# Kernel tuning notes

Measured on AMD Instinct MI355X. Metric: run time of the kernel, lower is better.

Reference implementation:

```python
import jax, jax.numpy as jnp
import numpy as np

B, D, N, MH, MV = 4, 1024, 2048, 1024, 1024

def setup_inputs() -> dict:
    key = jax.random.key(0)
    k1, k2, k3, k4, k5 = jax.random.split(key, 5)
    return {
        "x": jax.random.normal(k1, (B, D, N), dtype=jnp.float32),
        "W_Q": jax.random.normal(k2, (MH, D), dtype=jnp.float32),
        "W_K": jax.random.normal(k3, (MH, D), dtype=jnp.float32),
        "W_V": jax.random.normal(k4, (MV, D), dtype=jnp.float32),
        "W_O": jax.random.normal(k5, (D, MV), dtype=jnp.float32),
    }

def reference(x, W_Q, W_K, W_V, W_O):
    # x: [b, d, n] (feature-major). Projections: [b, m, n]
    q = jnp.einsum('hd,bdn->bhn', W_Q, x)
    k = jnp.einsum('hd,bdn->bhn', W_K, x)
    v = jnp.einsum('vd,bdn->bvn', W_V, x)
    # scores[b,i,j] = sum_h k[b,h,i] * q[b,h,j]  -> [b, n, n]; NOTE: no 1/sqrt scale (faithful)
    scores = jnp.einsum('bhi,bhj->bij', k, q)
    scores = jax.nn.softmax(scores, axis=-1)
    # v @ scores -> [b, m_V, n]
    attn = jnp.einsum('bvi,bij->bvj', v, scores)
    # W_O @ attn -> [b, d, n]
    return jnp.einsum('dv,bvj->bdj', W_O, attn)
```

## Files before the change

### kernel.cpp

```cpp
#include <hip/hip_runtime.h>
#include <cstddef>
#include <cstdint>

typedef unsigned short u16;
typedef __attribute__((ext_vector_type(8))) short bf16x8;
typedef __attribute__((ext_vector_type(8))) _Float16 f16x8;
typedef __attribute__((ext_vector_type(4))) float f32x4;
typedef __attribute__((ext_vector_type(16))) float f32x16;

#define GLOBAL_AS __attribute__((address_space(1)))
#define LDS_AS __attribute__((address_space(3)))

__device__ __forceinline__ void async16(const u16* g, u16* l) {
    __builtin_amdgcn_global_load_lds((GLOBAL_AS const uint32_t*)g,
                                     (LDS_AS uint32_t*)l, 16, 0, 0);
}

__device__ __forceinline__ u16 f2bf(float f) {
    uint32_t u = __builtin_bit_cast(uint32_t, f);
    uint32_t r = (u + 0x7FFFu + ((u >> 16) & 1u)) >> 16;
    return (u16)r;
}

#define VMC(N) asm volatile("s_waitcnt vmcnt(" #N ")" ::: "memory")

__global__ __launch_bounds__(256)
void wcast(const float4* __restrict__ src, u16* __restrict__ dst)
{
    int i = blockIdx.x * 256 + threadIdx.x;
    float4 v = src[i];
    ushort4 a = { f2bf(v.x), f2bf(v.y), f2bf(v.z), f2bf(v.w) };
    *(ushort4*)&dst[4 * (size_t)i] = a;
}

__global__ __launch_bounds__(256)
void tsplit_h2(const float* __restrict__ Sb, size_t sBatch,
               u16* __restrict__ Db, size_t dBatch, size_t plane,
               int R, int C)
{
    const float* S = Sb + blockIdx.z * sBatch;
    u16* D = Db + blockIdx.z * dBatch;
    __shared__ float t[32][33];
    int tx = threadIdx.x & 31, ty = threadIdx.x >> 5;
    int c0 = blockIdx.x * 32, r0 = blockIdx.y * 32;
    #pragma unroll
    for (int k = 0; k < 4; ++k)
        t[ty + 8 * k][tx] = S[(size_t)(r0 + ty + 8 * k) * C + c0 + tx];
    __syncthreads();
    #pragma unroll
    for (int k = 0; k < 4; ++k) {
        float a = t[tx][ty + 8 * k] * 64.0f;
        _Float16 h0 = (_Float16)a;
        _Float16 h1 = (_Float16)(a - (float)h0);
        size_t o = (size_t)(c0 + ty + 8 * k) * R + r0 + tx;
        D[o] = __builtin_bit_cast(u16, h0);
        D[plane + o] = __builtin_bit_cast(u16, h1);
    }
}

__global__ __launch_bounds__(256)
void xprep(const float* __restrict__ Sb, size_t sBatch,
           u16* __restrict__ BFb, size_t bfBatch,
           u16* __restrict__ Db, size_t dBatch, size_t plane)
{
    const float* S = Sb + blockIdx.z * sBatch;
    u16* BF = BFb + blockIdx.z * bfBatch;
    u16* D = Db + blockIdx.z * dBatch;
    __shared__ float t[32][33];
    int tx = threadIdx.x & 31, ty = threadIdx.x >> 5;
    int c0 = blockIdx.x * 32, r0 = blockIdx.y * 32;
    #pragma unroll
    for (int k = 0; k < 4; ++k) {
        float v = S[(size_t)(r0 + ty + 8 * k) * 2048 + c0 + tx];
        t[ty + 8 * k][tx] = v;
        BF[(size_t)(r0 + ty + 8 * k) * 2048 + c0 + tx] = f2bf(v);
    }
    __syncthreads();
    #pragma unroll
    for (int k = 0; k < 4; ++k) {
        float a = t[tx][ty + 8 * k] * 64.0f;
        _Float16 h0 = (_Float16)a;
        _Float16 h1 = (_Float16)(a - (float)h0);
        size_t o = (size_t)(c0 + ty + 8 * k) * 1024 + r0 + tx;
        D[o] = __builtin_bit_cast(u16, h0);
        D[plane + o] = __builtin_bit_cast(u16, h1);
    }
}

__global__ __launch_bounds__(256)
void tcast(const float* __restrict__ S, u16* __restrict__ D, int R, int C)
{
    __shared__ float t[32][33];
    int tx = threadIdx.x & 31, ty = threadIdx.x >> 5;
    int c0 = blockIdx.x * 32, r0 = blockIdx.y * 32;
    #pragma unroll
    for (int k = 0; k < 4; ++k)
        t[ty + 8 * k][tx] = S[(size_t)(r0 + ty + 8 * k) * C + c0 + tx];
    __syncthreads();
    #pragma unroll
    for (int k = 0; k < 4; ++k)
        D[(size_t)(c0 + ty + 8 * k) * R + r0 + tx] = f2bf(t[tx][ty + 8 * k]);
}

__global__ __launch_bounds__(256)
void tbf16(const u16* __restrict__ Sb, size_t sBatch, u16* __restrict__ Db, size_t dBatch)
{
    const u16* S = Sb + blockIdx.z * sBatch;
    u16* D = Db + blockIdx.z * dBatch;
    __shared__ u16 t[32][34];
    int tx = threadIdx.x & 31, ty = threadIdx.x >> 5;
    int c0 = blockIdx.x * 32, r0 = blockIdx.y * 32;
    #pragma unroll
    for (int k = 0; k < 4; ++k)
        t[ty + 8 * k][tx] = S[(size_t)(r0 + ty + 8 * k) * 2048 + c0 + tx];
    __syncthreads();
    #pragma unroll
    for (int k = 0; k < 4; ++k)
        D[(size_t)(c0 + ty + 8 * k) * 2048 + r0 + tx] = t[tx][ty + 8 * k];
}

#define MMF4(AF, BF)                                                                   \
    _Pragma("unroll") for (int i = 0; i < 4; ++i)                                      \
        _Pragma("unroll") for (int j = 0; j < 4; ++j)                                  \
            acc[i][j] = __builtin_amdgcn_mfma_f32_16x16x32_f16(AF[i], BF[j], acc[i][j], 0, 0, 0);
#define MMB4(AF, BF)                                                                   \
    _Pragma("unroll") for (int i = 0; i < 4; ++i)                                      \
        _Pragma("unroll") for (int j = 0; j < 4; ++j)                                  \
            acc[i][j] = __builtin_amdgcn_mfma_f32_16x16x32_bf16(AF[i], BF[j], acc[i][j], 0, 0, 0);

template<int TERMS, int EPI>
__global__ __launch_bounds__(256)
void gemm_big(const u16* __restrict__ Ab, size_t aBatch, size_t aPlane,
              const u16* __restrict__ Bb, size_t bBatch, size_t bPlane,
              void* __restrict__ Cb, size_t cBatch, size_t cPlane,
              int M, int N, int K)
{
    constexpr int RSZ = 4096;
    constexpr int BUF = (TERMS == 3 ? 4 : 2) * RSZ;
    __shared__ u16 lds[2 * BUF];
    const u16* A = Ab + blockIdx.z * aBatch;
    const u16* B = Bb + blockIdx.z * bBatch;
    const int tid = threadIdx.x;
    const int lane = tid & 63, wave = tid >> 6;
    const int m0 = blockIdx.y * 128, n0 = blockIdx.x * 128;
    const int l15 = lane & 15, q = lane >> 4;
    const int rm = (wave >> 1) * 64, rn = (wave & 1) * 64;

    int sr[2], sg[2], sbase[2];
    #pragma unroll
    for (int it = 0; it < 2; ++it) {
        int s = tid + it * 256;
        sr[it] = s >> 2;
        sg[it] = (s & 3) ^ ((sr[it] >> 1) & 3);
        sbase[it] = (it * 256 + wave * 64) * 8;
    }
    const int fsw = (q ^ ((l15 >> 1) & 3)) * 8;
    int aoff[4], boff[4];
    #pragma unroll
    for (int f = 0; f < 4; ++f) {
        aoff[f] = (rm + f * 16 + l15) * 32 + fsw;
        boff[f] = (rn + f * 16 + l15) * 32 + fsw;
    }

    f32x4 acc[4][4];
    #pragma unroll
    for (int i = 0; i < 4; ++i)
        #pragma unroll
        for (int j = 0; j < 4; ++j)
            acc[i][j] = (f32x4){0.f, 0.f, 0.f, 0.f};

#define STAGEB(PP, KT)                                                                 \
    do {                                                                               \
        _Pragma("unroll")                                                              \
        for (int it = 0; it < 2; ++it) {                                               \
            const size_t ao = (size_t)(m0 + sr[it]) * K + (KT) + sg[it] * 8;           \
            const size_t bo = (size_t)(n0 + sr[it]) * K + (KT) + sg[it] * 8;           \
            const int d = (PP) * BUF + sbase[it];                                      \
            if (TERMS == 3) {                                                          \
                async16(A + ao, &lds[d]);                                              \
                async16(A + aPlane + ao, &lds[d + RSZ]);                               \
                async16(B + bo, &lds[d + 2 * RSZ]);                                    \
                async16(B + bPlane + bo, &lds[d + 3 * RSZ]);                           \
            } else {                                                                   \
                async16(A + ao, &lds[d]);                                              \
                async16(B + bo, &lds[d + RSZ]);                                        \
            }                                                                          \
        }                                                                              \
    } while (0)

    STAGEB(0, 0);
    for (int kt = 0; kt < K; kt += 32) {
        const int p = (kt >> 5) & 1;
        __syncthreads();
        if (kt + 32 < K) STAGEB(p ^ 1, kt + 32);
        const u16* L = &lds[p * BUF];
        if (TERMS == 3) {
            f16x8 a0f[4], b0f[4], xf[4];
            #pragma unroll
            for (int f = 0; f < 4; ++f) a0f[f] = *(const f16x8*)&L[aoff[f]];
            #pragma unroll
            for (int f = 0; f < 4; ++f) b0f[f] = *(const f16x8*)&L[2 * RSZ + boff[f]];
            MMF4(a0f, b0f);
            #pragma unroll
            for (int f = 0; f < 4; ++f) xf[f] = *(const f16x8*)&L[3 * RSZ + boff[f]];
            MMF4(a0f, xf);
            #pragma unroll
            for (int f = 0; f < 4; ++f) xf[f] = *(const f16x8*)&L[RSZ + aoff[f]];
            MMF4(xf, b0f);
        } else {
            bf16x8 af[4], bf_[4];
            #pragma unroll
            for (int f = 0; f < 4; ++f) af[f] = *(const bf16x8*)&L[aoff[f]];
            #pragma unroll
            for (int f = 0; f < 4; ++f) bf_[f] = *(const bf16x8*)&L[RSZ + boff[f]];
            MMB4(af, bf_);
        }
    }
#undef STAGEB

    #pragma unroll
    for (int i = 0; i < 4; ++i) {
        int row = m0 + rm + i * 16 + q * 4;
        #pragma unroll
        for (int j = 0; j < 4; ++j) {
            int col = n0 + rn + j * 16 + l15;
            #pragma unroll
            for (int r = 0; r < 4; ++r) {
                float v = acc[i][j][r];
                size_t o = (size_t)(row + r) * N + col;
                if (EPI == 0) {
                    ((float*)Cb + blockIdx.z * cBatch)[o] = v;
                } else if (EPI == 1) {
                    u16* C0 = (u16*)Cb + blockIdx.z * cBatch;
                    float vs = v * 0.000244140625f;
                    _Float16 h0 = (_Float16)vs;
                    _Float16 h1 = (_Float16)(vs - (float)h0);
                    C0[o] = __builtin_bit_cast(u16, h0);
                    C0[cPlane + o] = __builtin_bit_cast(u16, h1);
                } else {
                    ((u16*)Cb + blockIdx.z * cBatch)[o] = f2bf(v);
                }
            }
        }
    }
}

template<int TERMS, int EPI, int TM, int TN, int WGM, int WGN>
__global__ __launch_bounds__(512, 2)
void gemm_w(const u16* __restrict__ Ab, size_t aBatch, size_t aPlane,
            const u16* __restrict__ Bb, size_t bBatch, size_t bPlane,
            void* __restrict__ Cb, size_t cBatch, size_t cPlane,
            int M, int N, int K)
{
    constexpr int ASZ = TM * 32;
    constexpr int BSZ = TN * 32;
    constexpr int APL = (TERMS == 3) ? 2 : 1;
    constexpr int BUF = APL * (ASZ + BSZ);
    constexpr int FM = TM / WGM / 32;
    constexpr int FN = TN / WGN / 32;
    constexpr int AIT = TM / 128;
    constexpr int BIT = TN / 128;
    extern __shared__ __align__(16) u16 lds[];

    int bid = blockIdx.x + gridDim.x * blockIdx.y;
    int cpr = gridDim.x >> 2;
    int c8 = bid & 7, kk = bid >> 3;
    int bx = (kk % cpr) * 4 + (c8 & 3);
    int by = (kk / cpr) * 2 + (c8 >> 2);

    const u16* A = Ab + blockIdx.z * aBatch;
    const u16* B = Bb + blockIdx.z * bBatch;
    const int tid = threadIdx.x;
    const int lane = tid & 63, wave = tid >> 6;
    const int m0 = by * TM, n0 = bx * TN;
    const int l31 = lane & 31, half = lane >> 5;
    const int rm = (wave / WGN) * (TM / WGM);
    const int rn = (wave % WGN) * (TN / WGN);

    int arow[FM], asw[FM], brow[FN], bsw[FN];
    #pragma unroll
    for (int f = 0; f < FM; ++f) { arow[f] = rm + f * 32 + l31; asw[f] = (arow[f] >> 1) & 3; }
    #pragma unroll
    for (int f = 0; f < FN; ++f) { brow[f] = rn + f * 32 + l31; bsw[f] = (brow[f] >> 1) & 3; }

    f32x16 acc[FM][FN];
    #pragma unroll
    for (int i = 0; i < FM; ++i)
        #pragma unroll
        for (int j = 0; j < FN; ++j)
            #pragma unroll
            for (int r = 0; r < 16; ++r) acc[i][j][r] = 0.f;

    auto stage = [&](int pp, int kt) {
        #pragma unroll
        for (int it = 0; it < AIT; ++it) {
            int s = tid + it * 512;
            int r = s >> 2;
            int g = (s & 3) ^ ((r >> 1) & 3);
            int base = pp * BUF + (it * 512 + wave * 64) * 8;
            size_t go = (size_t)(m0 + r) * K + kt + g * 8;
            async16(A + go, &lds[base]);
            if (TERMS == 3) async16(A + aPlane + go, &lds[base + ASZ]);
        }
        #pragma unroll
        for (int it = 0; it < BIT; ++it) {
            int s = tid + it * 512;
            int r = s >> 2;
            int g = (s & 3) ^ ((r >> 1) & 3);
            int base = pp * BUF + APL * ASZ + (it * 512 + wave * 64) * 8;
            size_t go = (size_t)(n0 + r) * K + kt + g * 8;
            async16(B + go, &lds[base]);
            if (TERMS == 3) async16(B + bPlane + go, &lds[base + BSZ]);
        }
    };

    stage(0, 0);
    for (int kt = 0; kt < K; kt += 32) {
        const int p = (kt >> 5) & 1;
        __syncthreads();
        if (kt + 32 < K) stage(p ^ 1, kt + 32);
        const u16* L = &lds[p * BUF];
        #pragma unroll
        for (int h = 0; h < 2; ++h) {
            bf16x8 a0[FM], b0[FN];
            #pragma unroll
            for (int f = 0; f < FM; ++f)
                a0[f] = *(const bf16x8*)&L[arow[f] * 32 + ((2 * h + half) ^ asw[f]) * 8];
            #pragma unroll
            for (int f = 0; f < FN; ++f)
                b0[f] = *(const bf16x8*)&L[ASZ + brow[f] * 32 + ((2 * h + half) ^ bsw[f]) * 8];
            #pragma unroll
            for (int i = 0; i < FM; ++i)
                #pragma unroll
                for (int j = 0; j < FN; ++j)
                    acc[i][j] = __builtin_amdgcn_mfma_f32_32x32x16_bf16(a0[i], b0[j], acc[i][j], 0, 0, 0);
        }
    }

    #pragma unroll
    for (int i = 0; i < FM; ++i) {
        #pragma unroll
        for (int j = 0; j < FN; ++j) {
            int col = n0 + rn + j * 32 + l31;
            #pragma unroll
            for (int r = 0; r < 16; ++r) {
                int row = m0 + rm + i * 32 + (r & 3) + 8 * (r >> 2) + 4 * half;
                float v = acc[i][j][r];
                size_t o = (size_t)row * N + col;
                if (EPI == 0) {
                    ((float*)Cb + blockIdx.z * cBatch)[o] = v;
                } else if (EPI == 1) {
                    u16* C0 = (u16*)Cb + blockIdx.z * cBatch;
                    float vs = v * 0.000244140625f;
                    _Float16 h0 = (_Float16)vs;
                    _Float16 h1 = (_Float16)(vs - (float)h0);
                    C0[o] = __builtin_bit_cast(u16, h0);
                    C0[cPlane + o] = __builtin_bit_cast(u16, h1);
                } else {
                    ((u16*)Cb + blockIdx.z * cBatch)[o] = f2bf(v);
                }
            }
        }
    }
}

template<int EPI, int TM, int TN, int WGM, int WGN>
__global__ __launch_bounds__(512, 2)
void gemm_p6(const u16* __restrict__ Ab, size_t aBatch, size_t aPlane,
             const u16* __restrict__ Bb, size_t bBatch, size_t bPlane,
             void* __restrict__ Cb, size_t cBatch, size_t cPlane,
             int M, int N, int K)
{
    constexpr int ASZ = TM * 32;
    constexpr int BSZ = TN * 32;
    constexpr int BUFU = 2 * (ASZ + BSZ);
    constexpr int FM = TM / WGM / 32;
    constexpr int FN = TN / WGN / 32;
    constexpr int LA = TM / 128;
    constexpr int LB = TN / 128;
    constexpr int NBND = LA + 2 * LB;
    static_assert(NBND == 6 || NBND == 4, "unexpected vmcnt constant");
    extern __shared__ __align__(16) u16 lds[];

    int bid = blockIdx.x + gridDim.x * blockIdx.y;
    int cpr = gridDim.x >> 2;
    int c8 = bid & 7, kk = bid >> 3;
    int bx = (kk % cpr) * 4 + (c8 & 3);
    int by = (kk / cpr) * 2 + (c8 >> 2);

    const u16* A = Ab + blockIdx.z * aBatch;
    const u16* B = Bb + blockIdx.z * bBatch;
    const int tid = threadIdx.x;
    const int lane = tid & 63, wave = tid >> 6;
    const int m0 = by * TM, n0 = bx * TN;
    const int l31 = lane & 31, half = lane >> 5;
    const int rm = (wave / WGN) * (TM / WGM);
    const int rn = (wave % WGN) * (TN / WGN);

    int arow[FM], asw[FM], brow[FN], bsw[FN];
    #pragma unroll
    for (int f = 0; f < FM; ++f) { arow[f] = rm + f * 32 + l31; asw[f] = (arow[f] >> 1) & 3; }
    #pragma unroll
    for (int f = 0; f < FN; ++f) { brow[f] = rn + f * 32 + l31; bsw[f] = (brow[f] >> 1) & 3; }

    f32x16 acc[FM][FN];
    #pragma unroll
    for (int i = 0; i < FM; ++i)
        #pragma unroll
        for (int j = 0; j < FN; ++j)
            #pragma unroll
            for (int r = 0; r < 16; ++r) acc[i][j][r] = 0.f;

    auto stA = [&](int t, const u16* sp, int uoff) {
        const int pp = (t & 1) * BUFU;
        const int kt = t << 5;
        #pragma unroll
        for (int it = 0; it < LA; ++it) {
            int s = tid + it * 512;
            int r = s >> 2;
            int g = (s & 3) ^ ((r >> 1) & 3);
            size_t go = (size_t)(m0 + r) * K + kt + g * 8;
            async16(sp + go, &lds[pp + uoff + (it * 512 + wave * 64) * 8]);
        }
    };
    auto stB = [&](int t, const u16* sp, int uoff) {
        const int pp = (t & 1) * BUFU;
        const int kt = t << 5;
        #pragma unroll
        for (int it = 0; it < LB; ++it) {
            int s = tid + it * 512;
            int r = s >> 2;
            int g = (s & 3) ^ ((r >> 1) & 3);
            size_t go = (size_t)(n0 + r) * K + kt + g * 8;
            async16(sp + go, &lds[pp + uoff + (it * 512 + wave * 64) * 8]);
        }
    };

    const int NT = K >> 5;

    stA(0, A, 0);
    stB(0, B, 2 * ASZ);
    stB(0, B + bPlane, 2 * ASZ + BSZ);
    stA(0, A + aPlane, ASZ);
    if (NT > 1) {
        stA(1, A, 0);
        stB(1, B, 2 * ASZ);
        stB(1, B + bPlane, 2 * ASZ + BSZ);
        if constexpr (NBND == 6) VMC(6); else VMC(4);
    } else {
        VMC(0);
    }
    __builtin_amdgcn_sched_barrier(0);
    __builtin_amdgcn_s_barrier();

    for (int t = 0; t < NT; ++t) {
        const u16* L = &lds[(t & 1) * BUFU];
        f16x8 a0r[FM][2], b0r[FN][2];

        #pragma unroll
        for (int h = 0; h < 2; ++h) {
            #pragma unroll
            for (int f = 0; f < FM; ++f)
                a0r[f][h] = *(const f16x8*)&L[arow[f] * 32 + ((2 * h + half) ^ asw[f]) * 8];
            #pragma unroll
            for (int f = 0; f < FN; ++f)
                b0r[f][h] = *(const f16x8*)&L[2 * ASZ + brow[f] * 32 + ((2 * h + half) ^ bsw[f]) * 8];
        }
        if (t + 1 < NT) stA(t + 1, A + aPlane, ASZ);
        __builtin_amdgcn_s_barrier();
        __builtin_amdgcn_s_setprio(1);
        #pragma unroll
        for (int h = 0; h < 2; ++h)
            #pragma unroll
            for (int i = 0; i < FM; ++i)
                #pragma unroll
                for (int j = 0; j < FN; ++j)
                    acc[i][j] = __builtin_amdgcn_mfma_f32_32x32x16_f16(a0r[i][h], b0r[j][h], acc[i][j], 0, 0, 0);
        __builtin_amdgcn_s_setprio(0);
        __builtin_amdgcn_s_barrier();

        {
            f16x8 tr[FN][2];
            #pragma unroll
            for (int h = 0; h < 2; ++h)
                #pragma unroll
                for (int f = 0; f < FN; ++f)
                    tr[f][h] = *(const f16x8*)&L[2 * ASZ + BSZ + brow[f] * 32 + ((2 * h + half) ^ bsw[f]) * 8];
            if (t + 2 < NT) { stA(t + 2, A, 0); stB(t + 2, B, 2 * ASZ); }
            __builtin_amdgcn_s_barrier();
            __builtin_amdgcn_s_setprio(1);
            #pragma unroll
            for (int h = 0; h < 2; ++h)
                #pragma unroll
                for (int i = 0; i < FM; ++i)
                    #pragma unroll
                    for (int j = 0; j < FN; ++j)
                        acc[i][j] = __builtin_amdgcn_mfma_f32_32x32x16_f16(a0r[i][h], tr[j][h], acc[i][j], 0, 0, 0);
            __builtin_amdgcn_s_setprio(0);
            __builtin_amdgcn_s_barrier();
        }

        {
            f16x8 tr[FM][2];
            #pragma unroll
            for (int h = 0; h < 2; ++h)
                #pragma unroll
                for (int f = 0; f < FM; ++f)
                    tr[f][h] = *(const f16x8*)&L[ASZ + arow[f] * 32 + ((2 * h + half) ^ asw[f]) * 8];
            if (t + 2 < NT) stB(t + 2, B + bPlane, 2 * ASZ + BSZ);
            __builtin_amdgcn_s_barrier();
            __builtin_amdgcn_s_setprio(1);
            #pragma unroll
            for (int h = 0; h < 2; ++h)
                #pragma unroll
                for (int i = 0; i < FM; ++i)
                    #pragma unroll
                    for (int j = 0; j < FN; ++j)
                        acc[i][j] = __builtin_amdgcn_mfma_f32_32x32x16_f16(tr[i][h], b0r[j][h], acc[i][j], 0, 0, 0);
            __builtin_amdgcn_s_setprio(0);
            if (t + 2 < NT) {
                if constexpr (NBND == 6) VMC(6); else VMC(4);
            } else if (t + 1 < NT) {
                VMC(0);
            }
            __builtin_amdgcn_sched_barrier(0);
            __builtin_amdgcn_s_barrier();
        }
    }

    #pragma unroll
    for (int i = 0; i < FM; ++i) {
        #pragma unroll
        for (int j = 0; j < FN; ++j) {
            int col = n0 + rn + j * 32 + l31;
            #pragma unroll
            for (int r = 0; r < 16; ++r) {
                int row = m0 + rm + i * 32 + (r & 3) + 8 * (r >> 2) + 4 * half;
                float v = acc[i][j][r];
                size_t o = (size_t)row * N + col;
                if (EPI == 0) {
                    ((float*)Cb + blockIdx.z * cBatch)[o] = v;
                } else if (EPI == 1) {
                    u16* C0 = (u16*)Cb + blockIdx.z * cBatch;
                    float vs = v * 0.000244140625f;
                    _Float16 h0 = (_Float16)vs;
                    _Float16 h1 = (_Float16)(vs - (float)h0);
                    C0[o] = __builtin_bit_cast(u16, h0);
                    C0[cPlane + o] = __builtin_bit_cast(u16, h1);
                } else {
                    ((u16*)Cb + blockIdx.z * cBatch)[o] = f2bf(v);
                }
            }
        }
    }
}

__global__ __launch_bounds__(256)
void softmax_p(const float* __restrict__ Sb, size_t sBatch, u16* __restrict__ Pb, size_t pBatch)
{
    const float* S = Sb + blockIdx.y * sBatch + (size_t)blockIdx.x * 2048;
    u16* P = Pb + blockIdx.y * pBatch + (size_t)blockIdx.x * 2048;
    const int tid = threadIdx.x;

    float4 v0 = *(const float4*)&S[tid * 4];
    float4 v1 = *(const float4*)&S[1024 + tid * 4];

    float m = fmaxf(fmaxf(fmaxf(v0.x, v0.y), fmaxf(v0.z, v0.w)),
                    fmaxf(fmaxf(v1.x, v1.y), fmaxf(v1.z, v1.w)));
    #pragma unroll
    for (int off = 32; off > 0; off >>= 1)
        m = fmaxf(m, __shfl_xor(m, off, 64));
    __shared__ float redm[4];
    if ((tid & 63) == 0) redm[tid >> 6] = m;
    __syncthreads();
    m = fmaxf(fmaxf(redm[0], redm[1]), fmaxf(redm[2], redm[3]));

    v0.x = __expf(v0.x - m); v0.y = __expf(v0.y - m);
    v0.z = __expf(v0.z - m); v0.w = __expf(v0.w - m);
    v1.x = __expf(v1.x - m); v1.y = __expf(v1.y - m);
    v1.z = __expf(v1.z - m); v1.w = __expf(v1.w - m);

    float s = v0.x + v0.y + v0.z + v0.w + v1.x + v1.y + v1.z + v1.w;
    #pragma unroll
    for (int off = 32; off > 0; off >>= 1)
        s += __shfl_xor(s, off, 64);
    __shared__ float reds[4];
    if ((tid & 63) == 0) reds[tid >> 6] = s;
    __syncthreads();
    s = reds[0] + reds[1] + reds[2] + reds[3];

    const float r = 1.0f / s;
    ushort4 o0 = { f2bf(v0.x * r), f2bf(v0.y * r), f2bf(v0.z * r), f2bf(v0.w * r) };
    ushort4 o1 = { f2bf(v1.x * r), f2bf(v1.y * r), f2bf(v1.z * r), f2bf(v1.w * r) };
    *(ushort4*)&P[tid * 4] = o0;
    *(ushort4*)&P[1024 + tid * 4] = o1;
}

extern "C" void kernel_launch(void* const* d_in, const int* in_sizes, int n_in,
                              void* d_out, int out_size, void* d_ws, size_t ws_size,
                              hipStream_t stream)
{
    const size_t MB = 1048576;
    const size_t WREG = 34 * MB;
    const size_t PER  = 32 * MB;
    const size_t PER_US = PER / 2, PER_F = PER / 4;

    char* ws = (char*)d_ws;
    u16* WQT2 = (u16*)ws;
    u16* WKT2 = (u16*)(ws + 4 * MB);
    u16* M2   = (u16*)(ws + 8 * MB);
    u16* WObf = (u16*)(ws + 12 * MB);
    u16* WVT  = (u16*)(ws + 14 * MB);
    u16* WOV  = (u16*)(ws + 16 * MB);
    u16* xbf  = (u16*)(ws + 18 * MB);

    int G = (ws_size >= WREG + 4 * PER) ? 4 : (ws_size >= WREG + 2 * PER) ? 2 : 1;

    const float* x = (const float*)d_in[0];
    float* out = (float*)d_out;
    dim3 blk(256);

    hipFuncSetAttribute((const void*)gemm_p6<0, 256, 256, 2, 4>,
                        hipFuncAttributeMaxDynamicSharedMemorySize, 131072);
    hipFuncSetAttribute((const void*)gemm_p6<1, 256, 128, 4, 2>,
                        hipFuncAttributeMaxDynamicSharedMemorySize, 98304);

    tsplit_h2<<<dim3(32, 32, 1), blk, 0, stream>>>((const float*)d_in[1], 0, WQT2, 0, 1048576, 1024, 1024);
    tsplit_h2<<<dim3(32, 32, 1), blk, 0, stream>>>((const float*)d_in[2], 0, WKT2, 0, 1048576, 1024, 1024);
    gemm_big<3, 1><<<dim3(8, 8, 1), blk, 0, stream>>>(WKT2, 0, 1048576, WQT2, 0, 1048576,
                                                      M2, 0, 1048576, 1024, 1024, 1024);
    wcast<<<1024, blk, 0, stream>>>((const float4*)d_in[4], WObf);
    tcast<<<dim3(32, 32, 1), blk, 0, stream>>>((const float*)d_in[3], WVT, 1024, 1024);
    gemm_big<1, 2><<<dim3(8, 8, 1), blk, 0, stream>>>(WObf, 0, 0, WVT, 0, 0,
                                                      WOV, 0, 0, 1024, 1024, 1024);

    for (int b0 = 0; b0 < 4; b0 += G) {
        char* R = ws + WREG;
        u16*   xT2 = (u16*)R;
        u16*   TT2 = (u16*)(R + 8 * MB);
        float* S32 = (float*)(R + 16 * MB);
        u16*   Pb  = (u16*)R;
        u16*   PTb = (u16*)(R + 8 * MB);
        u16*   XPT = (u16*)(R + 16 * MB);

        xprep<<<dim3(64, 32, G), blk, 0, stream>>>(x + (size_t)b0 * 2097152, 2097152,
                                                   xbf + (size_t)b0 * 2097152, 2097152,
                                                   xT2, PER_US, 2097152);
        gemm_p6<1, 256, 128, 4, 2><<<dim3(8, 8, G), 512, 98304, stream>>>(
            xT2, PER_US, 2097152, M2, 0, 1048576, TT2, PER_US, 2097152, 2048, 1024, 1024);
        gemm_p6<0, 256, 256, 2, 4><<<dim3(8, 8, G), 512, 131072, stream>>>(
            xT2, PER_US, 2097152, TT2, PER_US, 2097152, S32, PER_F, 0, 2048, 2048, 1024);
        softmax_p<<<dim3(2048, G), blk, 0, stream>>>(S32, PER_F, Pb, PER_US);
        tbf16<<<dim3(64, 64, G), blk, 0, stream>>>(Pb, PER_US, PTb, PER_US);
        gemm_w<1, 2, 256, 128, 4, 2><<<dim3(8, 8, G), 512, 49152, stream>>>(
            PTb, PER_US, 0, xbf + (size_t)b0 * 2097152, 2097152, 0,
            XPT, PER_US, 0, 2048, 1024, 2048);
        gemm_w<1, 0, 256, 128, 4, 2><<<dim3(16, 4, G), 512, 49152, stream>>>(
            WOV, 0, 0, XPT, PER_US, 0, out + (size_t)b0 * 2097152, 2097152, 0,
            1024, 2048, 1024);
    }
}
```

Before: 419.1 us.

## Replace gemm_p6 with simpler 128x128 double-buffered split-precision GEMM kernel

Replaces the hand-scheduled 512-thread gemm_p6, which used large tiles, manual vmcnt waits, setprio and many barriers, with gemm_s3. The new kernel uses 256 threads, 128x128 tiles and static LDS with one __syncthreads per k-step. The low-order A plane is now read straight from global memory into registers instead of being staged through LDS. The aim is a simpler pipeline with more blocks for occupancy and less LDS traffic. The cost is less data reuse per tile and uncoalesced direct global loads for one operand.

```diff
diff --git a/kernel.cpp b/kernel.cpp
--- a/kernel.cpp
+++ b/kernel.cpp
@@ -21,8 +21,6 @@
     uint32_t r = (u + 0x7FFFu + ((u >> 16) & 1u)) >> 16;
     return (u16)r;
 }
-
-#define VMC(N) asm volatile("s_waitcnt vmcnt(" #N ")" ::: "memory")
 
 __global__ __launch_bounds__(256)
 void wcast(const float4* __restrict__ src, u16* __restrict__ dst)
@@ -365,22 +363,20 @@
 }
 
 template<int EPI, int TM, int TN, int WGM, int WGN>
-__global__ __launch_bounds__(512, 2)
-void gemm_p6(const u16* __restrict__ Ab, size_t aBatch, size_t aPlane,
+__global__ __launch_bounds__(256, 2)
+void gemm_s3(const u16* __restrict__ Ab, size_t aBatch, size_t aPlane,
              const u16* __restrict__ Bb, size_t bBatch, size_t bPlane,
              void* __restrict__ Cb, size_t cBatch, size_t cPlane,
              int M, int N, int K)
 {
     constexpr int ASZ = TM * 32;
     constexpr int BSZ = TN * 32;
-    constexpr int BUFU = 2 * (ASZ + BSZ);
+    constexpr int BUF = ASZ + 2 * BSZ;
     constexpr int FM = TM / WGM / 32;
     constexpr int FN = TN / WGN / 32;
-    constexpr int LA = TM / 128;
-    constexpr int LB = TN / 128;
-    constexpr int NBND = LA + 2 * LB;
-    static_assert(NBND == 6 || NBND == 4, "unexpected vmcnt constant");
-    extern __shared__ __align__(16) u16 lds[];
+    constexpr int AIT = TM / 64;
+    constexpr int BIT = TN / 64;
+    __shared__ u16 lds[2 * BUF];
 
     int bid = blockIdx.x + gridDim.x * blockIdx.y;
     int cpr = gridDim.x >> 2;
@@ -390,6 +386,7 @@
 
     const u16* A = Ab + blockIdx.z * aBatch;
     const u16* B = Bb + blockIdx.z * bBatch;
+    const u16* A1 = A + aPlane;
     const int tid = threadIdx.x;
     const int lane = tid & 63, wave = tid >> 6;
     const int m0 = by * TM, n0 = bx * TN;
@@ -403,6 +400,10 @@
     #pragma unroll
     for (int f = 0; f < FN; ++f) { brow[f] = rn + f * 32 + l31; bsw[f] = (brow[f] >> 1) & 3; }
 
+    const u16* g1[FM];
+    #pragma unroll
+    for (int f = 0; f < FM; ++f) g1[f] = A1 + (size_t)(m0 + arow[f]) * K + half * 8;
+
     f32x16 acc[FM][FN];
     #pragma unroll
     for (int i = 0; i < FM; ++i)
@@ -411,121 +412,76 @@
             #pragma unroll
             for (int r = 0; r < 16; ++r) acc[i][j][r] = 0.f;
 
-    auto stA = [&](int t, const u16* sp, int uoff) {
-        const int pp = (t & 1) * BUFU;
-        const int kt = t << 5;
-        #pragma unroll
-        for (int it = 0; it < LA; ++it) {
-            int s = tid + it * 512;
+    auto stage = [&](int pp, int kt) {
+        #pragma unroll
+        for (int it = 0; it < AIT; ++it) {
+            int s = tid + it * 256;
             int r = s >> 2;
             int g = (s & 3) ^ ((r >> 1) & 3);
             size_t go = (size_t)(m0 + r) * K + kt + g * 8;
-            async16(sp + go, &lds[pp + uoff + (it * 512 + wave * 64) * 8]);
-        }
-    };
-    auto stB = [&](int t, const u16* sp, int uoff) {
-        const int pp = (t & 1) * BUFU;
-        const int kt = t << 5;
-        #pragma unroll
-        for (int it = 0; it < LB; ++it) {
-            int s = tid + it * 512;
+            async16(A + go, &lds[pp * BUF + (it * 256 + wave * 64) * 8]);
+        }
+        #pragma unroll
+        for (int it = 0; it < BIT; ++it) {
+            int s = tid + it * 256;
             int r = s >> 2;
             int g = (s & 3) ^ ((r >> 1) & 3);
             size_t go = (size_t)(n0 + r) * K + kt + g * 8;
-            async16(sp + go, &lds[pp + uoff + (it * 512 + wave * 64) * 8]);
+            async16(B + go, &lds[pp * BUF + ASZ + (it * 256 + wave * 64) * 8]);
+            async16(B + bPlane + go, &lds[pp * BUF + ASZ + BSZ + (it * 256 + wave * 64) * 8]);
         }
     };
 
-    const int NT = K >> 5;
-
-    stA(0, A, 0);
-    stB(0, B, 2 * ASZ);
-    stB(0, B + bPlane, 2 * ASZ + BSZ);
-    stA(0, A + aPlane, ASZ);
-    if (NT > 1) {
-        stA(1, A, 0);
-        stB(1, B, 2 * ASZ);
-        stB(1, B + bPlane, 2 * ASZ + BSZ);
-        if constexpr (NBND == 6) VMC(6); else VMC(4);
-    } else {
-        VMC(0);
-    }
-    __builtin_amdgcn_sched_barrier(0);
-    __builtin_amdgcn_s_barrier();
-
-    for (int t = 0; t < NT; ++t) {
-        const u16* L = &lds[(t & 1) * BUFU];
-        f16x8 a0r[FM][2], b0r[FN][2];
-
+    stage(0, 0);
+    for (int kt = 0; kt < K; kt += 32) {
+        const int p = (kt >> 5) & 1;
+        __syncthreads();
+        if (kt + 32 < K) stage(p ^ 1, kt + 32);
+
+        f16x8 a1g[2][FM];
+        #pragma unroll
+        for (int h = 0; h < 2; ++h)
+            #pragma unroll
+            for (int f = 0; f < FM; ++f)
+                a1g[h][f] = *(const f16x8*)&g1[f][kt + h * 16];
+
+        const u16* L = &lds[p * BUF];
+        f16x8 a0r[2][FM], b0r[2][FN];
         #pragma unroll
         for (int h = 0; h < 2; ++h) {
             #pragma unroll
             for (int f = 0; f < FM; ++f)
-                a0r[f][h] = *(const f16x8*)&L[arow[f] * 32 + ((2 * h + half) ^ asw[f]) * 8];
+                a0r[h][f] = *(const f16x8*)&L[arow[f] * 32 + ((2 * h + half) ^ asw[f]) * 8];
             #pragma unroll
             for (int f = 0; f < FN; ++f)
-                b0r[f][h] = *(const f16x8*)&L[2 * ASZ + brow[f] * 32 + ((2 * h + half) ^ bsw[f]) * 8];
-        }
-        if (t + 1 < NT) stA(t + 1, A + aPlane, ASZ);
-        __builtin_amdgcn_s_barrier();
-        __builtin_amdgcn_s_setprio(1);
+                b0r[h][f] = *(const f16x8*)&L[ASZ + brow[f] * 32 + ((2 * h + half) ^ bsw[f]) * 8];
+        }
         #pragma unroll
         for (int h = 0; h < 2; ++h)
             #pragma unroll
             for (int i = 0; i < FM; ++i)
                 #pragma unroll
                 for (int j = 0; j < FN; ++j)
-                    acc[i][j] = __builtin_amdgcn_mfma_f32_32x32x16_f16(a0r[i][h], b0r[j][h], acc[i][j], 0, 0, 0);
-        __builtin_amdgcn_s_setprio(0);
-        __builtin_amdgcn_s_barrier();
-
-        {
-            f16x8 tr[FN][2];
-            #pragma unroll
-            for (int h = 0; h < 2; ++h)
+                    acc[i][j] = __builtin_amdgcn_mfma_f32_32x32x16_f16(a0r[h][i], b0r[h][j], acc[i][j], 0, 0, 0);
+        #pragma unroll
+        for (int h = 0; h < 2; ++h) {
+            f16x8 b1r[FN];
+            #pragma unroll
+            for (int f = 0; f < FN; ++f)
+                b1r[f] = *(const f16x8*)&L[ASZ + BSZ + brow[f] * 32 + ((2 * h + half) ^ bsw[f]) * 8];
+            #pragma unroll
+            for (int i = 0; i < FM; ++i)
                 #pragma unroll
-                for (int f = 0; f < FN; ++f)
-                    tr[f][h] = *(const f16x8*)&L[2 * ASZ + BSZ + brow[f] * 32 + ((2 * h + half) ^ bsw[f]) * 8];
-            if (t + 2 < NT) { stA(t + 2, A, 0); stB(t + 2, B, 2 * ASZ); }
-            __builtin_amdgcn_s_barrier();
-            __builtin_amdgcn_s_setprio(1);
-            #pragma unroll
-            for (int h = 0; h < 2; ++h)
+                for (int j = 0; j < FN; ++j)
+                    acc[i][j] = __builtin_amdgcn_mfma_f32_32x32x16_f16(a0r[h][i], b1r[j], acc[i][j], 0, 0, 0);
+        }
+        #pragma unroll
+        for (int h = 0; h < 2; ++h)
+            #pragma unroll
+            for (int i = 0; i < FM; ++i)
                 #pragma unroll
-                for (int i = 0; i < FM; ++i)
-                    #pragma unroll
-                    for (int j = 0; j < FN; ++j)
-                        acc[i][j] = __builtin_amdgcn_mfma_f32_32x32x16_f16(a0r[i][h], tr[j][h], acc[i][j], 0, 0, 0);
-            __builtin_amdgcn_s_setprio(0);
-            __builtin_amdgcn_s_barrier();
-        }
-
-        {
-            f16x8 tr[FM][2];
-            #pragma unroll
-            for (int h = 0; h < 2; ++h)
-                #pragma unroll
-                for (int f = 0; f < FM; ++f)
-                    tr[f][h] = *(const f16x8*)&L[ASZ + arow[f] * 32 + ((2 * h + half) ^ asw[f]) * 8];
-            if (t + 2 < NT) stB(t + 2, B + bPlane, 2 * ASZ + BSZ);
-            __builtin_amdgcn_s_barrier();
-            __builtin_amdgcn_s_setprio(1);
-            #pragma unroll
-            for (int h = 0; h < 2; ++h)
-                #pragma unroll
-                for (int i = 0; i < FM; ++i)
-                    #pragma unroll
-                    for (int j = 0; j < FN; ++j)
-                        acc[i][j] = __builtin_amdgcn_mfma_f32_32x32x16_f16(tr[i][h], b0r[j][h], acc[i][j], 0, 0, 0);
-            __builtin_amdgcn_s_setprio(0);
-            if (t + 2 < NT) {
-                if constexpr (NBND == 6) VMC(6); else VMC(4);
-            } else if (t + 1 < NT) {
-                VMC(0);
-            }
-            __builtin_amdgcn_sched_barrier(0);
-            __builtin_amdgcn_s_barrier();
-        }
+                for (int j = 0; j < FN; ++j)
+                    acc[i][j] = __builtin_amdgcn_mfma_f32_32x32x16_f16(a1g[h][i], b0r[h][j], acc[i][j], 0, 0, 0);
     }
 
     #pragma unroll
@@ -620,11 +576,6 @@
     float* out = (float*)d_out;
     dim3 blk(256);
 
-    hipFuncSetAttribute((const void*)gemm_p6<0, 256, 256, 2, 4>,
-                        hipFuncAttributeMaxDynamicSharedMemorySize, 131072);
-    hipFuncSetAttribute((const void*)gemm_p6<1, 256, 128, 4, 2>,
-                        hipFuncAttributeMaxDynamicSharedMemorySize, 98304);
-
     tsplit_h2<<<dim3(32, 32, 1), blk, 0, stream>>>((const float*)d_in[1], 0, WQT2, 0, 1048576, 1024, 1024);
     tsplit_h2<<<dim3(32, 32, 1), blk, 0, stream>>>((const float*)d_in[2], 0, WKT2, 0, 1048576, 1024, 1024);
     gemm_big<3, 1><<<dim3(8, 8, 1), blk, 0, stream>>>(WKT2, 0, 1048576, WQT2, 0, 1048576,
@@ -646,9 +597,9 @@
         xprep<<<dim3(64, 32, G), blk, 0, stream>>>(x + (size_t)b0 * 2097152, 2097152,
                                                    xbf + (size_t)b0 * 2097152, 2097152,
                                                    xT2, PER_US, 2097152);
-        gemm_p6<1, 256, 128, 4, 2><<<dim3(8, 8, G), 512, 98304, stream>>>(
+        gemm_s3<1, 128, 128, 2, 2><<<dim3(8, 16, G), blk, 0, stream>>>(
             xT2, PER_US, 2097152, M2, 0, 1048576, TT2, PER_US, 2097152, 2048, 1024, 1024);
-        gemm_p6<0, 256, 256, 2, 4><<<dim3(8, 8, G), 512, 131072, stream>>>(
+        gemm_s3<0, 128, 128, 2, 2><<<dim3(16, 16, G), blk, 0, stream>>>(
             xT2, PER_US, 2097152, TT2, PER_US, 2097152, S32, PER_F, 0, 2048, 2048, 1024);
         softmax_p<<<dim3(2048, G), blk, 0, stream>>>(S32, PER_F, Pb, PER_US);
         tbf16<<<dim3(64, 64, G), blk, 0, stream>>>(Pb, PER_US, PTb, PER_US);
```

Measured after the change: 443.5 us. 5.8% more time.
